# Optimization experiments

Measured on AMD Instinct MI355X. Metric: run time of the kernel, lower is better.

## Reference

```python
import jax, jax.numpy as jnp
import numpy as np

N = 50000
K = 32
C = 256  # hidden_dim

def setup_inputs() -> dict:
    key = jax.random.key(0)
    k1, k2, k3, k4 = jax.random.split(key, 4)
    feat = jax.random.normal(k1, (N, C), dtype=jnp.float32)
    coords = jax.random.normal(k2, (N, 3), dtype=jnp.float32)
    knn_idx = jax.random.randint(k3, (N, K), 0, N, dtype=jnp.int32)
    # Dense(hidden_dim) over concat([feat(C), agg(C), rel_mean(3), rel_std(3)]) -> in_dim = 2C + 6
    W = jax.random.normal(k4, (2 * C + 6, C), dtype=jnp.float32) * (1.0 / np.sqrt(2 * C + 6))
    b = jnp.zeros((C,), dtype=jnp.float32)
    return {"feat": feat, "coords": coords, "knn_idx": knn_idx, "W": W, "b": b}

def reference(feat, coords, knn_idx, W, b):
    # Neighbor feature aggregation: gather (N,K,C) then mean over K
    nbr_feat = feat[knn_idx]                      # (N, K, C)
    agg = jnp.mean(nbr_feat, axis=1)              # (N, C)
    # Relative coordinate statistics
    nbr_coords = coords[knn_idx]                  # (N, K, 3)
    rel = nbr_coords - coords[:, None, :]         # (N, K, 3)
    rel_mean = jnp.mean(rel, axis=1)              # (N, 3)
    rel_var = jnp.mean(jnp.square(rel), axis=1) - jnp.square(rel_mean)
    rel_std = jnp.sqrt(jnp.maximum(rel_var, 0.0))  # population std, like tf.math.reduce_std
    mix = jnp.concatenate([feat, agg, rel_mean, rel_std], axis=-1)  # (N, 2C+6)
    out = jax.nn.silu(mix @ W + b)                # (N, C)
    return out
```

## Files before the change

### kernel.cpp

```cpp
#include <hip/hip_runtime.h>
#include <math.h>


typedef __attribute__((ext_vector_type(8))) short short8;
typedef __attribute__((ext_vector_type(4))) float f32x4;
typedef __attribute__((ext_vector_type(2))) float f32x2;

constexpr int K = 32;
constexpr int C = 256;
constexpr int IN_DIM = 2 * C + 6;
constexpr int KP = 544;
constexpr int BM = 32;
constexpr int MIXS = 552;
constexpr int NT = 256;

__device__ __forceinline__ unsigned short f2bf(float f) {
  union { float f; unsigned u; } c; c.f = f;
  return (unsigned short)((c.u + 0x7fffu + ((c.u >> 16) & 1u)) >> 16);
}
__device__ __forceinline__ unsigned pack2(float lo, float hi) {
  return (unsigned)f2bf(lo) | ((unsigned)f2bf(hi) << 16);
}

__global__ __launch_bounds__(256) void prep_feat_q(const float* __restrict__ feat,
                                                   uint2* __restrict__ featq,
                                                   long total8) {
  long i = (long)blockIdx.x * 256 + threadIdx.x;
  if (i < total8) {
    const float4 v0 = reinterpret_cast<const float4*>(feat)[2 * i];
    const float4 v1 = reinterpret_cast<const float4*>(feat)[2 * i + 1];
    unsigned a = 0, b = 0;
    a = __builtin_amdgcn_cvt_pk_fp8_f32(v0.x, v0.y, a, false);
    a = __builtin_amdgcn_cvt_pk_fp8_f32(v0.z, v0.w, a, true);
    b = __builtin_amdgcn_cvt_pk_fp8_f32(v1.x, v1.y, b, false);
    b = __builtin_amdgcn_cvt_pk_fp8_f32(v1.z, v1.w, b, true);
    uint2 o; o.x = a; o.y = b;
    featq[i] = o;
  }
}

__global__ __launch_bounds__(256) void prep_w(const float* __restrict__ W,
                                              unsigned short* __restrict__ Wt) {
  int i = blockIdx.x * 256 + threadIdx.x;
  if (i < C * KP) {
    int nn = i / KP, k = i - nn * KP;
    float v = (k < IN_DIM) ? W[(size_t)k * C + nn] : 0.f;
    Wt[i] = f2bf(v);
  }
}

__global__ __launch_bounds__(NT, 4)
void gcl_main(const unsigned char* __restrict__ featq,
              const float* __restrict__ feat,
              const float* __restrict__ coords,
              const int*   __restrict__ knn,
              const unsigned short* __restrict__ Wt,
              const float* __restrict__ bias,
              float* __restrict__ out, int n)
{
  __shared__ unsigned short mix[BM][MIXS];
  __shared__ int knnLds[BM * K];

  const int t = threadIdx.x;
  const int row0 = blockIdx.x * BM;

  #pragma unroll
  for (int i = 0; i < (BM * K) / NT; ++i) {
    int e = t + i * NT;
    int r = e >> 5, k = e & 31;
    int g = row0 + r; if (g >= n) g = n - 1;
    knnLds[e] = knn[(size_t)g * K + k];
  }
  for (int e = t; e < BM * (KP - IN_DIM); e += NT) {
    int r = e / (KP - IN_DIM), c = e - r * (KP - IN_DIM);
    mix[r][IN_DIM + c] = 0;
  }
  __syncthreads();

  const int w    = t >> 6;
  const int lane = t & 63;
  const int cl   = lane & 15;
  const int rq   = lane >> 4;

  #pragma unroll
  for (int p = 0; p < 2; ++p) {
    const int r = (w << 3) + (p << 2) + rq;
    int g = row0 + r; if (g >= n) g = n - 1;

    {
      const float4 s0 = *reinterpret_cast<const float4*>(feat + (size_t)g * C + cl * 16 + 0);
      const float4 s1 = *reinterpret_cast<const float4*>(feat + (size_t)g * C + cl * 16 + 4);
      const float4 s2 = *reinterpret_cast<const float4*>(feat + (size_t)g * C + cl * 16 + 8);
      const float4 s3 = *reinterpret_cast<const float4*>(feat + (size_t)g * C + cl * 16 + 12);
      uint4 o0, o1;
      o0.x = pack2(s0.x, s0.y); o0.y = pack2(s0.z, s0.w);
      o0.z = pack2(s1.x, s1.y); o0.w = pack2(s1.z, s1.w);
      o1.x = pack2(s2.x, s2.y); o1.y = pack2(s2.z, s2.w);
      o1.z = pack2(s3.x, s3.y); o1.w = pack2(s3.z, s3.w);
      *reinterpret_cast<uint4*>(&mix[r][cl * 16 + 0]) = o0;
      *reinterpret_cast<uint4*>(&mix[r][cl * 16 + 8]) = o1;
    }

    const int* ids = &knnLds[r * K];
    float a0=0,a1=0,a2=0,a3=0,a4=0,a5=0,a6=0,a7=0;
    float a8=0,a9=0,aA=0,aB=0,aC=0,aD=0,aE=0,aF=0;
    #pragma unroll 8
    for (int k = 0; k < K; ++k) {
      const uint4 v = *reinterpret_cast<const uint4*>(featq + (size_t)ids[k] * C + cl * 16);
      f32x2 d0 = __builtin_amdgcn_cvt_pk_f32_fp8(v.x, false);
      f32x2 d1 = __builtin_amdgcn_cvt_pk_f32_fp8(v.x, true);
      f32x2 d2 = __builtin_amdgcn_cvt_pk_f32_fp8(v.y, false);
      f32x2 d3 = __builtin_amdgcn_cvt_pk_f32_fp8(v.y, true);
      f32x2 d4 = __builtin_amdgcn_cvt_pk_f32_fp8(v.z, false);
      f32x2 d5 = __builtin_amdgcn_cvt_pk_f32_fp8(v.z, true);
      f32x2 d6 = __builtin_amdgcn_cvt_pk_f32_fp8(v.w, false);
      f32x2 d7 = __builtin_amdgcn_cvt_pk_f32_fp8(v.w, true);
      a0 += d0.x; a1 += d0.y; a2 += d1.x; a3 += d1.y;
      a4 += d2.x; a5 += d2.y; a6 += d3.x; a7 += d3.y;
      a8 += d4.x; a9 += d4.y; aA += d5.x; aB += d5.y;
      aC += d6.x; aD += d6.y; aE += d7.x; aF += d7.y;
    }
    const float s = 1.0f / 32.0f;
    uint4 o0, o1;
    o0.x = pack2(a0 * s, a1 * s); o0.y = pack2(a2 * s, a3 * s);
    o0.z = pack2(a4 * s, a5 * s); o0.w = pack2(a6 * s, a7 * s);
    o1.x = pack2(a8 * s, a9 * s); o1.y = pack2(aA * s, aB * s);
    o1.z = pack2(aC * s, aD * s); o1.w = pack2(aE * s, aF * s);
    *reinterpret_cast<uint4*>(&mix[r][C + cl * 16 + 0]) = o0;
    *reinterpret_cast<uint4*>(&mix[r][C + cl * 16 + 8]) = o1;
  }

  if (t < BM * 3) {
    const int r = t / 3, d = t - r * 3;
    int g = row0 + r; if (g >= n) g = n - 1;
    const int* ids = &knnLds[r * K];
    float s = 0.f, ss = 0.f;
    #pragma unroll 8
    for (int k = 0; k < K; ++k) {
      float v = coords[(size_t)ids[k] * 3 + d];
      s += v; ss += v * v;
    }
    const float m = s * (1.0f / 32.0f);
    const float var = ss * (1.0f / 32.0f) - m * m;
    mix[r][2 * C + d]     = f2bf(m - coords[(size_t)g * 3 + d]);
    mix[r][2 * C + 3 + d] = f2bf(sqrtf(fmaxf(var, 0.f)));
  }
  __syncthreads();

  const int n0  = w * 64;
  const int l15 = lane & 15;
  const int h   = lane >> 4;

  f32x4 acc[2][4];
  #pragma unroll
  for (int mt = 0; mt < 2; ++mt)
    #pragma unroll
    for (int nt = 0; nt < 4; ++nt)
      acc[mt][nt] = (f32x4){0.f, 0.f, 0.f, 0.f};

  const unsigned short* wbase = Wt + (size_t)(n0 + l15) * KP + 8 * h;

  #pragma unroll 1
  for (int s8 = 0; s8 < KP / 32; ++s8) {
    const int kb = s8 * 32;
    short8 A0 = *reinterpret_cast<const short8*>(&mix[l15][kb + 8 * h]);
    short8 A1 = *reinterpret_cast<const short8*>(&mix[16 + l15][kb + 8 * h]);
    short8 B0 = *reinterpret_cast<const short8*>(wbase + 0 * 16 * KP + kb);
    short8 B1 = *reinterpret_cast<const short8*>(wbase + 1 * 16 * KP + kb);
    short8 B2 = *reinterpret_cast<const short8*>(wbase + 2 * 16 * KP + kb);
    short8 B3 = *reinterpret_cast<const short8*>(wbase + 3 * 16 * KP + kb);
    acc[0][0] = __builtin_amdgcn_mfma_f32_16x16x32_bf16(A0, B0, acc[0][0], 0, 0, 0);
    acc[1][0] = __builtin_amdgcn_mfma_f32_16x16x32_bf16(A1, B0, acc[1][0], 0, 0, 0);
    acc[0][1] = __builtin_amdgcn_mfma_f32_16x16x32_bf16(A0, B1, acc[0][1], 0, 0, 0);
    acc[1][1] = __builtin_amdgcn_mfma_f32_16x16x32_bf16(A1, B1, acc[1][1], 0, 0, 0);
    acc[0][2] = __builtin_amdgcn_mfma_f32_16x16x32_bf16(A0, B2, acc[0][2], 0, 0, 0);
    acc[1][2] = __builtin_amdgcn_mfma_f32_16x16x32_bf16(A1, B2, acc[1][2], 0, 0, 0);
    acc[0][3] = __builtin_amdgcn_mfma_f32_16x16x32_bf16(A0, B3, acc[0][3], 0, 0, 0);
    acc[1][3] = __builtin_amdgcn_mfma_f32_16x16x32_bf16(A1, B3, acc[1][3], 0, 0, 0);
  }

  #pragma unroll
  for (int mt = 0; mt < 2; ++mt) {
    #pragma unroll
    for (int nt = 0; nt < 4; ++nt) {
      const int col = n0 + nt * 16 + l15;
      const float bv = bias[col];
      f32x4 a = acc[mt][nt];
      #pragma unroll
      for (int q = 0; q < 4; ++q) {
        const int grow = row0 + mt * 16 + 4 * h + q;
        if (grow < n) {
          const float x = a[q] + bv;
          out[(size_t)grow * C + col] = x / (1.f + __expf(-x));
        }
      }
    }
  }
}

constexpr int MIX_STRIDE = 520;

#define FMA4(mcomp, wv)                                                        \
  a.x = fmaf((mcomp), (wv).x, a.x);                                            \
  a.y = fmaf((mcomp), (wv).y, a.y);                                            \
  a.z = fmaf((mcomp), (wv).z, a.z);                                            \
  a.w = fmaf((mcomp), (wv).w, a.w);

__global__ __launch_bounds__(256, 2)
void gcl_fused(const float* __restrict__ feat,
               const float* __restrict__ coords,
               const int*   __restrict__ knn,
               const float* __restrict__ W,
               const float* __restrict__ bias,
               float* __restrict__ out,
               int n)
{
  __shared__ float mix[BM][MIX_STRIDE];
  __shared__ int   knnLds[BM * K];

  const int t = threadIdx.x;
  const int row0 = blockIdx.x * BM;

  #pragma unroll
  for (int i = 0; i < (BM * K) / 256; ++i) {
    const int e = t + i * 256;
    const int r = e >> 5;
    const int k = e & (K - 1);
    int grow = row0 + r; if (grow >= n) grow = n - 1;
    knnLds[e] = knn[(size_t)grow * K + k];
  }
  __syncthreads();

  const int c4 = t & 63;
  const int rg = t >> 6;

  for (int ri = 0; ri < BM / 4; ++ri) {
    const int r = rg * (BM / 4) + ri;
    int grow = row0 + r; if (grow >= n) grow = n - 1;
    const int* ids = &knnLds[r * K];
    float sx = 0.f, sy = 0.f, sz = 0.f, sw = 0.f;
    #pragma unroll 8
    for (int k = 0; k < K; ++k) {
      const float4 f = *reinterpret_cast<const float4*>(feat + (size_t)ids[k] * C + c4 * 4);
      sx += f.x; sy += f.y; sz += f.z; sw += f.w;
    }
    const float4 self = *reinterpret_cast<const float4*>(feat + (size_t)grow * C + c4 * 4);
    float* mr = mix[r];
    *reinterpret_cast<float4*>(mr + c4 * 4) = self;
    const float inv = 1.0f / (float)K;
    float4 a; a.x = sx * inv; a.y = sy * inv; a.z = sz * inv; a.w = sw * inv;
    *reinterpret_cast<float4*>(mr + C + c4 * 4) = a;
  }

  if (t < BM * 3) {
    const int r = t / 3;
    const int d = t - r * 3;
    int grow = row0 + r; if (grow >= n) grow = n - 1;
    const int* ids = &knnLds[r * K];
    float s = 0.f, ss = 0.f;
    #pragma unroll 8
    for (int k = 0; k < K; ++k) {
      const float v = coords[(size_t)ids[k] * 3 + d];
      s += v; ss += v * v;
    }
    const float inv = 1.0f / (float)K;
    const float m = s * inv;
    const float var = ss * inv - m * m;
    mix[r][2 * C + d]     = m - coords[(size_t)grow * 3 + d];
    mix[r][2 * C + 3 + d] = sqrtf(fmaxf(var, 0.f));
  }
  __syncthreads();

  const int c0 = (t & 63) * 4;
  const int rbase = rg * (BM / 4);

  float4 acc[BM / 4];
  {
    const float4 bv = *reinterpret_cast<const float4*>(bias + c0);
    #pragma unroll
    for (int ri = 0; ri < BM / 4; ++ri) acc[ri] = bv;
  }

  for (int jb = 0; jb < 129; ++jb) {
    const int j = jb * 4;
    const float4 w0 = *reinterpret_cast<const float4*>(W + (size_t)(j + 0) * C + c0);
    const float4 w1 = *reinterpret_cast<const float4*>(W + (size_t)(j + 1) * C + c0);
    const float4 w2 = *reinterpret_cast<const float4*>(W + (size_t)(j + 2) * C + c0);
    const float4 w3 = *reinterpret_cast<const float4*>(W + (size_t)(j + 3) * C + c0);
    #pragma unroll
    for (int ri = 0; ri < BM / 4; ++ri) {
      const float4 m4 = *reinterpret_cast<const float4*>(&mix[rbase + ri][j]);
      float4 a = acc[ri];
      FMA4(m4.x, w0)
      FMA4(m4.y, w1)
      FMA4(m4.z, w2)
      FMA4(m4.w, w3)
      acc[ri] = a;
    }
  }
  #pragma unroll
  for (int jt = IN_DIM - 2; jt < IN_DIM; ++jt) {
    const float4 wv = *reinterpret_cast<const float4*>(W + (size_t)jt * C + c0);
    #pragma unroll
    for (int ri = 0; ri < BM / 4; ++ri) {
      const float m = mix[rbase + ri][jt];
      float4 a = acc[ri];
      FMA4(m, wv)
      acc[ri] = a;
    }
  }

  #pragma unroll
  for (int ri = 0; ri < BM / 4; ++ri) {
    const int grow = row0 + rbase + ri;
    if (grow < n) {
      float4 a = acc[ri];
      a.x = a.x / (1.f + expf(-a.x));
      a.y = a.y / (1.f + expf(-a.y));
      a.z = a.z / (1.f + expf(-a.z));
      a.w = a.w / (1.f + expf(-a.w));
      *reinterpret_cast<float4*>(out + (size_t)grow * C + c0) = a;
    }
  }
}

extern "C" void kernel_launch(void* const* d_in, const int* in_sizes, int n_in,
                              void* d_out, int out_size, void* d_ws, size_t ws_size,
                              hipStream_t stream) {
  const float* feat   = (const float*)d_in[0];
  const float* coords = (const float*)d_in[1];
  const int*   knn    = (const int*)d_in[2];
  const float* W      = (const float*)d_in[3];
  const float* bias   = (const float*)d_in[4];
  float* out = (float*)d_out;

  const int n = in_sizes[0] / C;
  const int grid = (n + BM - 1) / BM;

  const size_t featq_bytes = (size_t)n * C;
  const size_t wt_bytes    = (size_t)C * KP * 2;

  if (ws_size >= featq_bytes + wt_bytes) {
    unsigned char* featq  = (unsigned char*)d_ws;
    unsigned short* Wt    = (unsigned short*)((char*)d_ws + featq_bytes);
    const long total8 = (long)n * C / 8;
    hipLaunchKernelGGL(prep_feat_q, dim3((unsigned)((total8 + 255) / 256)), dim3(256), 0, stream,
                       feat, (uint2*)featq, total8);
    hipLaunchKernelGGL(prep_w, dim3((C * KP + 255) / 256), dim3(256), 0, stream, W, Wt);
    hipLaunchKernelGGL(gcl_main, dim3(grid), dim3(NT), 0, stream,
                       featq, feat, coords, knn, Wt, bias, out, n);
  } else {
    hipLaunchKernelGGL(gcl_fused, dim3(grid), dim3(256), 0, stream,
                       feat, coords, knn, W, bias, out, n);
  }
}
```

Baseline: 126.6 us.

## Halve row tile to 16 and parallelize coord stats with wave shuffles

```diff
diff --git a/kernel.cpp b/kernel.cpp
--- a/kernel.cpp
+++ b/kernel.cpp
@@ -10,7 +10,7 @@
 constexpr int C = 256;
 constexpr int IN_DIM = 2 * C + 6;
 constexpr int KP = 544;
-constexpr int BM = 32;
+constexpr int BM = 16;
 constexpr int MIXS = 552;
 constexpr int NT = 256;
 
@@ -49,7 +49,7 @@
   }
 }
 
-__global__ __launch_bounds__(NT, 4)
+__global__ __launch_bounds__(NT, 8)
 void gcl_main(const unsigned char* __restrict__ featq,
               const float* __restrict__ feat,
               const float* __restrict__ coords,
@@ -82,9 +82,8 @@
   const int cl   = lane & 15;
   const int rq   = lane >> 4;
 
-  #pragma unroll
-  for (int p = 0; p < 2; ++p) {
-    const int r = (w << 3) + (p << 2) + rq;
+  {
+    const int r = (w << 2) + rq;
     int g = row0 + r; if (g >= n) g = n - 1;
 
     {
@@ -130,20 +129,35 @@
     *reinterpret_cast<uint4*>(&mix[r][C + cl * 16 + 8]) = o1;
   }
 
-  if (t < BM * 3) {
-    const int r = t / 3, d = t - r * 3;
-    int g = row0 + r; if (g >= n) g = n - 1;
-    const int* ids = &knnLds[r * K];
-    float s = 0.f, ss = 0.f;
-    #pragma unroll 8
-    for (int k = 0; k < K; ++k) {
-      float v = coords[(size_t)ids[k] * 3 + d];
-      s += v; ss += v * v;
-    }
-    const float m = s * (1.0f / 32.0f);
-    const float var = ss * (1.0f / 32.0f) - m * m;
-    mix[r][2 * C + d]     = f2bf(m - coords[(size_t)g * 3 + d]);
-    mix[r][2 * C + 3 + d] = f2bf(sqrtf(fmaxf(var, 0.f)));
+  #pragma unroll
+  for (int pass = 0; pass < 2; ++pass) {
+    const int sr = (t >> 5) + pass * 8;
+    const int sk = t & 31;
+    const int id = knnLds[sr * K + sk];
+    const float x = coords[(size_t)id * 3 + 0];
+    const float y = coords[(size_t)id * 3 + 1];
+    const float z = coords[(size_t)id * 3 + 2];
+    float sx = x, sy = y, sz = z;
+    float qx = x * x, qy = y * y, qz = z * z;
+    #pragma unroll
+    for (int m = 1; m < 32; m <<= 1) {
+      sx += __shfl_xor(sx, m); sy += __shfl_xor(sy, m); sz += __shfl_xor(sz, m);
+      qx += __shfl_xor(qx, m); qy += __shfl_xor(qy, m); qz += __shfl_xor(qz, m);
+    }
+    if (sk == 0) {
+      int g = row0 + sr; if (g >= n) g = n - 1;
+      const float inv = 1.0f / 32.0f;
+      const float mx = sx * inv, my = sy * inv, mz = sz * inv;
+      const float vx = qx * inv - mx * mx;
+      const float vy = qy * inv - my * my;
+      const float vz = qz * inv - mz * mz;
+      mix[sr][2 * C + 0] = f2bf(mx - coords[(size_t)g * 3 + 0]);
+      mix[sr][2 * C + 1] = f2bf(my - coords[(size_t)g * 3 + 1]);
+      mix[sr][2 * C + 2] = f2bf(mz - coords[(size_t)g * 3 + 2]);
+      mix[sr][2 * C + 3] = f2bf(sqrtf(fmaxf(vx, 0.f)));
+      mix[sr][2 * C + 4] = f2bf(sqrtf(fmaxf(vy, 0.f)));
+      mix[sr][2 * C + 5] = f2bf(sqrtf(fmaxf(vz, 0.f)));
+    }
   }
   __syncthreads();
 
@@ -151,12 +165,9 @@
   const int l15 = lane & 15;
   const int h   = lane >> 4;
 
-  f32x4 acc[2][4];
-  #pragma unroll
-  for (int mt = 0; mt < 2; ++mt)
-    #pragma unroll
-    for (int nt = 0; nt < 4; ++nt)
-      acc[mt][nt] = (f32x4){0.f, 0.f, 0.f, 0.f};
+  f32x4 acc[4];
+  #pragma unroll
+  for (int nt = 0; nt < 4; ++nt) acc[nt] = (f32x4){0.f, 0.f, 0.f, 0.f};
 
   const unsigned short* wbase = Wt + (size_t)(n0 + l15) * KP + 8 * h;
 
@@ -164,40 +175,33 @@
   for (int s8 = 0; s8 < KP / 32; ++s8) {
     const int kb = s8 * 32;
     short8 A0 = *reinterpret_cast<const short8*>(&mix[l15][kb + 8 * h]);
-    short8 A1 = *reinterpret_cast<const short8*>(&mix[16 + l15][kb + 8 * h]);
     short8 B0 = *reinterpret_cast<const short8*>(wbase + 0 * 16 * KP + kb);
     short8 B1 = *reinterpret_cast<const short8*>(wbase + 1 * 16 * KP + kb);
     short8 B2 = *reinterpret_cast<const short8*>(wbase + 2 * 16 * KP + kb);
     short8 B3 = *reinterpret_cast<const short8*>(wbase + 3 * 16 * KP + kb);
-    acc[0][0] = __builtin_amdgcn_mfma_f32_16x16x32_bf16(A0, B0, acc[0][0], 0, 0, 0);
-    acc[1][0] = __builtin_amdgcn_mfma_f32_16x16x32_bf16(A1, B0, acc[1][0], 0, 0, 0);
-    acc[0][1] = __builtin_amdgcn_mfma_f32_16x16x32_bf16(A0, B1, acc[0][1], 0, 0, 0);
-    acc[1][1] = __builtin_amdgcn_mfma_f32_16x16x32_bf16(A1, B1, acc[1][1], 0, 0, 0);
-    acc[0][2] = __builtin_amdgcn_mfma_f32_16x16x32_bf16(A0, B2, acc[0][2], 0, 0, 0);
-    acc[1][2] = __builtin_amdgcn_mfma_f32_16x16x32_bf16(A1, B2, acc[1][2], 0, 0, 0);
-    acc[0][3] = __builtin_amdgcn_mfma_f32_16x16x32_bf16(A0, B3, acc[0][3], 0, 0, 0);
-    acc[1][3] = __builtin_amdgcn_mfma_f32_16x16x32_bf16(A1, B3, acc[1][3], 0, 0, 0);
-  }
-
-  #pragma unroll
-  for (int mt = 0; mt < 2; ++mt) {
-    #pragma unroll
-    for (int nt = 0; nt < 4; ++nt) {
-      const int col = n0 + nt * 16 + l15;
-      const float bv = bias[col];
-      f32x4 a = acc[mt][nt];
-      #pragma unroll
-      for (int q = 0; q < 4; ++q) {
-        const int grow = row0 + mt * 16 + 4 * h + q;
-        if (grow < n) {
-          const float x = a[q] + bv;
-          out[(size_t)grow * C + col] = x / (1.f + __expf(-x));
-        }
+    acc[0] = __builtin_amdgcn_mfma_f32_16x16x32_bf16(A0, B0, acc[0], 0, 0, 0);
+    acc[1] = __builtin_amdgcn_mfma_f32_16x16x32_bf16(A0, B1, acc[1], 0, 0, 0);
+    acc[2] = __builtin_amdgcn_mfma_f32_16x16x32_bf16(A0, B2, acc[2], 0, 0, 0);
+    acc[3] = __builtin_amdgcn_mfma_f32_16x16x32_bf16(A0, B3, acc[3], 0, 0, 0);
+  }
+
+  #pragma unroll
+  for (int nt = 0; nt < 4; ++nt) {
+    const int col = n0 + nt * 16 + l15;
+    const float bv = bias[col];
+    f32x4 a = acc[nt];
+    #pragma unroll
+    for (int q = 0; q < 4; ++q) {
+      const int grow = row0 + 4 * h + q;
+      if (grow < n) {
+        const float x = a[q] + bv;
+        out[(size_t)grow * C + col] = x / (1.f + __expf(-x));
       }
     }
   }
 }
 
+constexpr int BMF = 32;
 constexpr int MIX_STRIDE = 520;
 
 #define FMA4(mcomp, wv)                                                        \
@@ -215,14 +219,14 @@
                float* __restrict__ out,
                int n)
 {
-  __shared__ float mix[BM][MIX_STRIDE];
-  __shared__ int   knnLds[BM * K];
+  __shared__ float mix[BMF][MIX_STRIDE];
+  __shared__ int   knnLds[BMF * K];
 
   const int t = threadIdx.x;
-  const int row0 = blockIdx.x * BM;
-
-  #pragma unroll
-  for (int i = 0; i < (BM * K) / 256; ++i) {
+  const int row0 = blockIdx.x * BMF;
+
+  #pragma unroll
+  for (int i = 0; i < (BMF * K) / 256; ++i) {
     const int e = t + i * 256;
     const int r = e >> 5;
     const int k = e & (K - 1);
@@ -234,8 +238,8 @@
   const int c4 = t & 63;
   const int rg = t >> 6;
 
-  for (int ri = 0; ri < BM / 4; ++ri) {
-    const int r = rg * (BM / 4) + ri;
+  for (int ri = 0; ri < BMF / 4; ++ri) {
+    const int r = rg * (BMF / 4) + ri;
     int grow = row0 + r; if (grow >= n) grow = n - 1;
     const int* ids = &knnLds[r * K];
     float sx = 0.f, sy = 0.f, sz = 0.f, sw = 0.f;
@@ -252,7 +256,7 @@
     *reinterpret_cast<float4*>(mr + C + c4 * 4) = a;
   }
 
-  if (t < BM * 3) {
+  if (t < BMF * 3) {
     const int r = t / 3;
     const int d = t - r * 3;
     int grow = row0 + r; if (grow >= n) grow = n - 1;
@@ -272,13 +276,13 @@
   __syncthreads();
 
   const int c0 = (t & 63) * 4;
-  const int rbase = rg * (BM / 4);
-
-  float4 acc[BM / 4];
+  const int rbase = rg * (BMF / 4);
+
+  float4 acc[BMF / 4];
   {
     const float4 bv = *reinterpret_cast<const float4*>(bias + c0);
     #pragma unroll
-    for (int ri = 0; ri < BM / 4; ++ri) acc[ri] = bv;
+    for (int ri = 0; ri < BMF / 4; ++ri) acc[ri] = bv;
   }
 
   for (int jb = 0; jb < 129; ++jb) {
@@ -288,7 +292,7 @@
     const float4 w2 = *reinterpret_cast<const float4*>(W + (size_t)(j + 2) * C + c0);
     const float4 w3 = *reinterpret_cast<const float4*>(W + (size_t)(j + 3) * C + c0);
     #pragma unroll
-    for (int ri = 0; ri < BM / 4; ++ri) {
+    for (int ri = 0; ri < BMF / 4; ++ri) {
       const float4 m4 = *reinterpret_cast<const float4*>(&mix[rbase + ri][j]);
       float4 a = acc[ri];
       FMA4(m4.x, w0)
@@ -302,7 +306,7 @@
   for (int jt = IN_DIM - 2; jt < IN_DIM; ++jt) {
     const float4 wv = *reinterpret_cast<const float4*>(W + (size_t)jt * C + c0);
     #pragma unroll
-    for (int ri = 0; ri < BM / 4; ++ri) {
+    for (int ri = 0; ri < BMF / 4; ++ri) {
       const float m = mix[rbase + ri][jt];
       float4 a = acc[ri];
       FMA4(m, wv)
@@ -311,7 +315,7 @@
   }
 
   #pragma unroll
-  for (int ri = 0; ri < BM / 4; ++ri) {
+  for (int ri = 0; ri < BMF / 4; ++ri) {
     const int grow = row0 + rbase + ri;
     if (grow < n) {
       float4 a = acc[ri];
@@ -335,7 +339,6 @@
   float* out = (float*)d_out;
 
   const int n = in_sizes[0] / C;
-  const int grid = (n + BM - 1) / BM;
 
   const size_t featq_bytes = (size_t)n * C;
   const size_t wt_bytes    = (size_t)C * KP * 2;
@@ -344,13 +347,15 @@
     unsigned char* featq  = (unsigned char*)d_ws;
     unsigned short* Wt    = (unsigned short*)((char*)d_ws + featq_bytes);
     const long total8 = (long)n * C / 8;
+    const int grid = (n + BM - 1) / BM;
     hipLaunchKernelGGL(prep_feat_q, dim3((unsigned)((total8 + 255) / 256)), dim3(256), 0, stream,
                        feat, (uint2*)featq, total8);
     hipLaunchKernelGGL(prep_w, dim3((C * KP + 255) / 256), dim3(256), 0, stream, W, Wt);
     hipLaunchKernelGGL(gcl_main, dim3(grid), dim3(NT), 0, stream,
                        featq, feat, coords, knn, Wt, bias, out, n);
   } else {
-    hipLaunchKernelGGL(gcl_fused, dim3(grid), dim3(256), 0, stream,
+    const int gridf = (n + BMF - 1) / BMF;
+    hipLaunchKernelGGL(gcl_fused, dim3(gridf), dim3(256), 0, stream,
                        feat, coords, knn, W, bias, out, n);
   }
 }
```

Result: slower. 133.8 us (+5.7%).
